# Performance work log

Measured on AMD Instinct MI355X. Metric: run time of the kernel, lower is better.

Reference implementation:

```python
import jax, jax.numpy as jnp
import numpy as np

B, S, D, H = 2, 4096, 768, 12
DEPTH = D // H


def setup_inputs() -> dict:
    key = jax.random.key(0)
    ks = jax.random.split(key, 6)
    return {
        "q": jax.random.normal(ks[0], (B, S, D), dtype=jnp.float32),
        "k": jax.random.normal(ks[1], (B, S, D), dtype=jnp.float32),
        "v": jax.random.normal(ks[2], (B, S, D), dtype=jnp.float32),
        "wq": jax.random.normal(ks[3], (D, D), dtype=jnp.float32),
        "wk": jax.random.normal(ks[4], (D, D), dtype=jnp.float32),
        "wv": jax.random.normal(ks[5], (D, D), dtype=jnp.float32),
    }


def _split_heads(x):
    # [B, S, D] -> [B, H, S, depth]
    b, s, _ = x.shape
    return x.reshape(b, s, H, DEPTH).transpose(0, 2, 1, 3)


def reference(q, k, v, wq, wk, wv):
    qh = _split_heads(q @ wq)  # [B,H,S,dh]
    kh = _split_heads(k @ wk)
    vh = _split_heads(v @ wv)
    scale = 1.0 / jnp.sqrt(jnp.asarray(DEPTH, dtype=qh.dtype))
    scores = jnp.einsum("bhqd,bhkd->bhqk", qh, kh) * scale  # [B,H,S,S]
    attn = jax.nn.softmax(scores, axis=-1)
    out = jnp.einsum("bhqk,bhkd->bhqd", attn, vh)  # [B,H,S,dh]
    return out.transpose(0, 2, 1, 3).reshape(q.shape[0], -1, D)
```

## Files before the change

kernel.cpp:

```cpp
#include <hip/hip_runtime.h>
#include <cstdint>

#define B_   2
#define S_   4096
#define D_   768
#define H_   12
#define DH_  64
#define BH_  (B_*H_)
#define M_   (B_*S_)
#define SCALE 0.125f

typedef _Float16 fp16;
typedef __attribute__((ext_vector_type(8))) _Float16 fp16x8;
typedef __attribute__((ext_vector_type(4))) _Float16 fp16x4;
typedef __attribute__((ext_vector_type(4))) float    f32x4;

#define MFMA16(a,b,c) __builtin_amdgcn_mfma_f32_16x16x32_f16((a),(b),(c),0,0,0)

__device__ __forceinline__ void gld_lds16(const void* g, void* l) {
  __builtin_amdgcn_global_load_lds(
      (const __attribute__((address_space(1))) unsigned int*)g,
      (__attribute__((address_space(3))) unsigned int*)l, 16, 0, 0);
}

__device__ __forceinline__ void stage64x128(const char* gbase, int pitch,
                                            char* lds, int tid) {
  const int lane = tid & 63, wv = tid >> 6;
#pragma unroll
  for (int j = 0; j < 2; ++j) {
    const int o   = (wv*2 + j)*1024 + lane*16;
    const int row = o >> 7;
    const int cb  = (o & 127) ^ ((row & 7) << 4);
    gld_lds16(gbase + (size_t)row*pitch + cb, lds + (wv*2 + j)*1024);
  }
}

__device__ __forceinline__ fp16x8 lds_h8(const char* base, int row, int cb) {
  return *(const fp16x8*)(base + row*128 + (cb ^ ((row & 7) << 4)));
}

__global__ __launch_bounds__(256) void prep_w(const float* __restrict__ wq,
                                              const float* __restrict__ wk,
                                              const float* __restrict__ wv,
                                              fp16* __restrict__ wt) {
  const int idx = blockIdx.x*256 + threadIdx.x;
  const int mat = idx / (768*768);
  const int e   = idx % (768*768);
  const int n   = e / 768, k = e % 768;
  const float* w = mat == 0 ? wq : (mat == 1 ? wk : wv);
  const float v = w[(size_t)k*768 + n];
  fp16* base = wt + (size_t)mat * (2*768*768);
  const fp16 hv = (fp16)v;
  base[e]            = hv;
  base[768*768 + e]  = (fp16)(v - (float)hv);
}

__global__ __launch_bounds__(256) void proj_gemm(
    const float* __restrict__ xq, const float* __restrict__ xk,
    const float* __restrict__ xv, const fp16* __restrict__ wt,
    fp16* __restrict__ qhi, fp16* __restrict__ qlo,
    fp16* __restrict__ khi, fp16* __restrict__ klo,
    fp16* __restrict__ vtp) {
  __shared__ __align__(16) char sm[16384];
  char* sWh = sm;
  char* sWl = sm + 8192;
  const int tid = threadIdx.x, lane = tid & 63, wv = tid >> 6;
  const int c = lane & 15, g = lane >> 4;
  const int mb  = blockIdx.x * 64;
  const int h   = blockIdx.y;
  const int nb  = h * 64;
  const int mat = blockIdx.z;
  const float* x = mat == 0 ? xq : (mat == 1 ? xk : xv);
  const fp16* wth = wt + (size_t)mat * (2*768*768);
  const fp16* wtl = wth + 768*768;

  f32x4 acc[4] = {};
  const int xrow = mb + wv*16 + c;

  for (int k0 = 0; k0 < 768; k0 += 64) {
    __syncthreads();
    stage64x128((const char*)(wth + (size_t)nb*768 + k0), 768*2, sWh, tid);
    stage64x128((const char*)(wtl + (size_t)nb*768 + k0), 768*2, sWl, tid);
    __syncthreads();

    fp16x8 ah[2], al[2];
#pragma unroll
    for (int ks = 0; ks < 2; ++ks) {
      const float* xp = x + (size_t)xrow*768 + k0 + ks*32 + g*8;
      const f32x4 x0 = *(const f32x4*)xp;
      const f32x4 x1 = *(const f32x4*)(xp + 4);
#pragma unroll
      for (int j = 0; j < 8; ++j) {
        const float v = j < 4 ? x0[j] : x1[j - 4];
        const fp16 hv = (fp16)v;
        ah[ks][j] = hv;
        al[ks][j] = (fp16)(v - (float)hv);
      }
    }
#pragma unroll
    for (int ks = 0; ks < 2; ++ks)
#pragma unroll
      for (int nt = 0; nt < 4; ++nt) {
        const fp16x8 bh = lds_h8(sWh, nt*16 + c, ks*64 + g*16);
        const fp16x8 bl = lds_h8(sWl, nt*16 + c, ks*64 + g*16);
        acc[nt] = MFMA16(ah[ks], bh, acc[nt]);
        acc[nt] = MFMA16(ah[ks], bl, acc[nt]);
        acc[nt] = MFMA16(al[ks], bh, acc[nt]);
      }
  }

  if (mat < 2) {
    fp16* ph = mat ? khi : qhi;
    fp16* pl = mat ? klo : qlo;
#pragma unroll
    for (int nt = 0; nt < 4; ++nt)
#pragma unroll
      for (int r = 0; r < 4; ++r) {
        const int m = mb + wv*16 + g*4 + r;
        const int bb = m >> 12, s = m & (S_-1);
        const size_t idx = ((size_t)(bb*H_ + h)*S_ + s)*DH_ + nt*16 + c;
        const float v = acc[nt][r];
        const fp16 hv = (fp16)v;
        ph[idx] = hv;
        pl[idx] = (fp16)(v - (float)hv);
      }
  } else {
    __syncthreads();
    fp16* tile = (fp16*)sm;
#pragma unroll
    for (int nt = 0; nt < 4; ++nt) {
      const int dd = nt*16 + c, ml = wv*16 + g*4;
      const fp16x4 hv = {(fp16)acc[nt][0], (fp16)acc[nt][1],
                         (fp16)acc[nt][2], (fp16)acc[nt][3]};
      *(fp16x4*)(tile + dd*64 + ml) = hv;
    }
    __syncthreads();
    const int bb = mb >> 12, s0 = mb & (S_-1);
    const int dd = tid >> 2, ml0 = (tid & 3) * 16;
    const size_t obase = ((size_t)(bb*H_ + h)*DH_ + dd)*S_ + s0 + ml0;
#pragma unroll
    for (int u = 0; u < 2; ++u)
      *(fp16x8*)(vtp + obase + u*8) = *(const fp16x8*)(tile + dd*64 + ml0 + u*8);
  }
}

__global__ __launch_bounds__(256) void mha_flash(
    const fp16* __restrict__ qhi, const fp16* __restrict__ qlo,
    const fp16* __restrict__ khi, const fp16* __restrict__ klo,
    const fp16* __restrict__ vt, float* __restrict__ out) {
  __shared__ __align__(16) char sm[49152];
  char* sQh = sm;
  char* sQl = sm + 8192;
  char* sKh = sm + 16384;
  char* sKl = sm + 24576;
  char* sV  = sm + 32768;
  char* sP  = sm + 40960;

  const int tid = threadIdx.x, lane = tid & 63, wv = tid >> 6;
  const int c = lane & 15, g = lane >> 4;
  const int qb = blockIdx.x * 64;
  const int bh = blockIdx.y;
  const int b = bh / H_, h = bh % H_;

  const size_t qoff = ((size_t)bh*S_ + qb) * DH_;
  stage64x128((const char*)(qhi + qoff), 128, sQh, tid);
  stage64x128((const char*)(qlo + qoff), 128, sQl, tid);
  __syncthreads();

  fp16x8 qfh[2], qfl[2];
#pragma unroll
  for (int ks = 0; ks < 2; ++ks) {
    qfh[ks] = lds_h8(sQh, wv*16 + c, ks*64 + g*16);
    qfl[ks] = lds_h8(sQl, wv*16 + c, ks*64 + g*16);
  }

  float m_run = -1e30f, l_run = 0.f;
  f32x4 accO[4] = {};

  for (int kt = 0; kt < S_/64; ++kt) {
    const int kvb = kt * 64;
    __syncthreads();
    const size_t koff = ((size_t)bh*S_ + kvb) * DH_;
    stage64x128((const char*)(khi + koff), 128, sKh, tid);
    stage64x128((const char*)(klo + koff), 128, sKl, tid);
    stage64x128((const char*)(vt + (size_t)bh*DH_*S_ + kvb), S_*2, sV, tid);
    __syncthreads();

    f32x4 accS[4] = {};
#pragma unroll
    for (int t = 0; t < 4; ++t)
#pragma unroll
      for (int ks = 0; ks < 2; ++ks) {
        const fp16x8 kfh = lds_h8(sKh, t*16 + c, ks*64 + g*16);
        const fp16x8 kfl = lds_h8(sKl, t*16 + c, ks*64 + g*16);
        accS[t] = MFMA16(kfh, qfh[ks], accS[t]);
        accS[t] = MFMA16(kfh, qfl[ks], accS[t]);
        accS[t] = MFMA16(kfl, qfh[ks], accS[t]);
      }

    float mx = -1e30f;
#pragma unroll
    for (int t = 0; t < 4; ++t)
#pragma unroll
      for (int r = 0; r < 4; ++r) mx = fmaxf(mx, accS[t][r]);
    mx = fmaxf(mx, __shfl_xor(mx, 16));
    mx = fmaxf(mx, __shfl_xor(mx, 32));
    const float m_new = fmaxf(m_run, mx);
    const float corr = __expf((m_run - m_new) * SCALE);
    float psum = 0.f;
#pragma unroll
    for (int t = 0; t < 4; ++t)
#pragma unroll
      for (int r = 0; r < 4; ++r) {
        const float p = __expf((accS[t][r] - m_new) * SCALE);
        accS[t][r] = p;
        psum += p;
      }
    psum += __shfl_xor(psum, 16);
    psum += __shfl_xor(psum, 32);
    l_run = l_run * corr + psum;
    m_run = m_new;

    char* pbase = sP + wv*2048;
#pragma unroll
    for (int t = 0; t < 4; ++t) {
      const fp16x4 pw = {(fp16)accS[t][0], (fp16)accS[t][1],
                         (fp16)accS[t][2], (fp16)accS[t][3]};
      *(fp16x4*)(pbase + c*128 + ((t*32 + g*8) ^ ((c & 7) << 4))) = pw;
    }

    float cr[4];
#pragma unroll
    for (int r = 0; r < 4; ++r)
      cr[r] = __shfl(corr, (lane & 48) | (g*4 + r));
#pragma unroll
    for (int d = 0; d < 4; ++d)
#pragma unroll
      for (int r = 0; r < 4; ++r) accO[d][r] *= cr[r];

#pragma unroll
    for (int ks = 0; ks < 2; ++ks) {
      const fp16x8 pf = *(const fp16x8*)(pbase + c*128 +
                                         ((ks*64 + g*16) ^ ((c & 7) << 4)));
#pragma unroll
      for (int d = 0; d < 4; ++d) {
        const fp16x8 vf = lds_h8(sV, d*16 + c, ks*64 + g*16);
        accO[d] = MFMA16(pf, vf, accO[d]);
      }
    }
  }

  float inv[4];
#pragma unroll
  for (int r = 0; r < 4; ++r)
    inv[r] = 1.f / __shfl(l_run, (lane & 48) | (g*4 + r));
  const int s0 = qb + wv*16 + g*4;
#pragma unroll
  for (int d = 0; d < 4; ++d)
#pragma unroll
    for (int r = 0; r < 4; ++r)
      out[((size_t)(b*S_ + s0 + r))*D_ + h*DH_ + d*16 + c] = accO[d][r] * inv[r];
}

extern "C" void kernel_launch(void* const* d_in, const int* in_sizes, int n_in,
                              void* d_out, int out_size, void* d_ws, size_t ws_size,
                              hipStream_t stream) {
  const float* xq = (const float*)d_in[0];
  const float* xk = (const float*)d_in[1];
  const float* xv = (const float*)d_in[2];
  const float* wq = (const float*)d_in[3];
  const float* wk = (const float*)d_in[4];
  const float* wv = (const float*)d_in[5];
  float* out = (float*)d_out;

  fp16* wt  = (fp16*)d_ws;
  fp16* qhi = wt + (size_t)6*768*768;
  const size_t PL = (size_t)BH_*S_*DH_;
  fp16* qlo = qhi + PL;
  fp16* khi = qlo + PL;
  fp16* klo = khi + PL;
  fp16* vtp = klo + PL;

  hipLaunchKernelGGL(prep_w, dim3(3*768*768/256), dim3(256), 0, stream,
                     wq, wk, wv, wt);
  hipLaunchKernelGGL(proj_gemm, dim3(M_/64, H_, 3), dim3(256), 0, stream,
                     xq, xk, xv, wt, qhi, qlo, khi, klo, vtp);
  hipLaunchKernelGGL(mha_flash, dim3(S_/64, BH_), dim3(256), 0, stream,
                     qhi, qlo, khi, klo, vtp, out);
}
```

Before: 524.2 us.

## Double query rows per flash block and streamline softmax with exp2 and lazy rescale

The attention kernel now handles 128 query rows per block (32 per wave) instead of 64, so each staged K/V tile is reused across twice as many queries. The grid is halved to match. Softmax switches to hardware exp2 with a pre-folded scale, packs probabilities with cvt_pkrtz, and skips the accumulator rescale when no row max grows. Row sums are computed with an MFMA against a ones vector instead of shuffles. LDS swizzle offsets are precomputed per lane. The costs are higher register pressure and fewer blocks per launch, and rounding the sum from fp16 P rather than fp32 slightly changes numerics.

```diff
diff --git a/kernel.cpp b/kernel.cpp
--- a/kernel.cpp
+++ b/kernel.cpp
@@ -8,7 +8,6 @@
 #define DH_  64
 #define BH_  (B_*H_)
 #define M_   (B_*S_)
-#define SCALE 0.125f
 
 typedef _Float16 fp16;
 typedef __attribute__((ext_vector_type(8))) _Float16 fp16x8;
@@ -16,6 +15,14 @@
 typedef __attribute__((ext_vector_type(4))) float    f32x4;
 
 #define MFMA16(a,b,c) __builtin_amdgcn_mfma_f32_16x16x32_f16((a),(b),(c),0,0,0)
+
+__device__ __forceinline__ float exp2_hw(float x) {
+  float r; asm("v_exp_f32 %0, %1" : "=v"(r) : "v"(x)); return r;
+}
+__device__ __forceinline__ uint32_t pkrtz(float a, float b) {
+  uint32_t r; asm("v_cvt_pkrtz_f16_f32 %0, %1, %2" : "=v"(r) : "v"(a), "v"(b));
+  return r;
+}
 
 __device__ __forceinline__ void gld_lds16(const void* g, void* l) {
   __builtin_amdgcn_global_load_lds(
@@ -33,10 +40,6 @@
     const int cb  = (o & 127) ^ ((row & 7) << 4);
     gld_lds16(gbase + (size_t)row*pitch + cb, lds + (wv*2 + j)*1024);
   }
-}
-
-__device__ __forceinline__ fp16x8 lds_h8(const char* base, int row, int cb) {
-  return *(const fp16x8*)(base + row*128 + (cb ^ ((row & 7) << 4)));
 }
 
 __global__ __launch_bounds__(256) void prep_w(const float* __restrict__ wq,
@@ -66,6 +69,9 @@
   char* sWl = sm + 8192;
   const int tid = threadIdx.x, lane = tid & 63, wv = tid >> 6;
   const int c = lane & 15, g = lane >> 4;
+  const int r128 = c * 128;
+  const int co0 = ((c & 7) ^ g) << 4;
+  const int co1 = co0 ^ 64;
   const int mb  = blockIdx.x * 64;
   const int h   = blockIdx.y;
   const int nb  = h * 64;
@@ -79,8 +85,8 @@
 
   for (int k0 = 0; k0 < 768; k0 += 64) {
     __syncthreads();
-    stage64x128((const char*)(wth + (size_t)nb*768 + k0), 768*2, sWh, tid);
-    stage64x128((const char*)(wtl + (size_t)nb*768 + k0), 768*2, sWl, tid);
+    stage64x128((const char*)(wth + (size_t)nb*768 + k0), 1536, sWh, tid);
+    stage64x128((const char*)(wtl + (size_t)nb*768 + k0), 1536, sWl, tid);
     __syncthreads();
 
     fp16x8 ah[2], al[2];
@@ -101,8 +107,11 @@
     for (int ks = 0; ks < 2; ++ks)
 #pragma unroll
       for (int nt = 0; nt < 4; ++nt) {
-        const fp16x8 bh = lds_h8(sWh, nt*16 + c, ks*64 + g*16);
-        const fp16x8 bl = lds_h8(sWl, nt*16 + c, ks*64 + g*16);
+        const char* wb  = sWh + r128 + nt*2048;
+        const char* wlb = sWl + r128 + nt*2048;
+        const int co = ks ? co1 : co0;
+        const fp16x8 bh = *(const fp16x8*)(wb  + co);
+        const fp16x8 bl = *(const fp16x8*)(wlb + co);
         acc[nt] = MFMA16(ah[ks], bh, acc[nt]);
         acc[nt] = MFMA16(ah[ks], bl, acc[nt]);
         acc[nt] = MFMA16(al[ks], bh, acc[nt]);
@@ -148,118 +157,169 @@
     const fp16* __restrict__ qhi, const fp16* __restrict__ qlo,
     const fp16* __restrict__ khi, const fp16* __restrict__ klo,
     const fp16* __restrict__ vt, float* __restrict__ out) {
-  __shared__ __align__(16) char sm[49152];
-  char* sQh = sm;
-  char* sQl = sm + 8192;
-  char* sKh = sm + 16384;
-  char* sKl = sm + 24576;
-  char* sV  = sm + 32768;
-  char* sP  = sm + 40960;
+  __shared__ __align__(16) char sm[40960];
+  char* sKh = sm;
+  char* sKl = sm + 8192;
+  char* sV  = sm + 16384;
+  char* sP  = sm + 24576;
 
   const int tid = threadIdx.x, lane = tid & 63, wv = tid >> 6;
   const int c = lane & 15, g = lane >> 4;
-  const int qb = blockIdx.x * 64;
+  const int r128 = c * 128;
+  const int co0 = ((c & 7) ^ g) << 4;
+  const int co1 = co0 ^ 64;
+  const int pg3 = (g & 1) << 3;
+  const int pse = ((c & 7) ^ (g >> 1)) << 4;
+  const int qb = blockIdx.x * 128;
   const int bh = blockIdx.y;
   const int b = bh / H_, h = bh % H_;
 
   const size_t qoff = ((size_t)bh*S_ + qb) * DH_;
-  stage64x128((const char*)(qhi + qoff), 128, sQh, tid);
-  stage64x128((const char*)(qlo + qoff), 128, sQl, tid);
+  stage64x128((const char*)(qhi + qoff),          128, sm,         tid);
+  stage64x128((const char*)(qhi + qoff + 64*DH_), 128, sm +  8192, tid);
+  stage64x128((const char*)(qlo + qoff),          128, sm + 16384, tid);
+  stage64x128((const char*)(qlo + qoff + 64*DH_), 128, sm + 24576, tid);
   __syncthreads();
 
-  fp16x8 qfh[2], qfl[2];
-#pragma unroll
-  for (int ks = 0; ks < 2; ++ks) {
-    qfh[ks] = lds_h8(sQh, wv*16 + c, ks*64 + g*16);
-    qfl[ks] = lds_h8(sQl, wv*16 + c, ks*64 + g*16);
-  }
-
-  float m_run = -1e30f, l_run = 0.f;
-  f32x4 accO[4] = {};
+  fp16x8 qfh[2][2], qfl[2][2];
+  {
+    const char* hb = sm + (wv >> 1)*8192;
+    const char* lb = sm + 16384 + (wv >> 1)*8192;
+#pragma unroll
+    for (int qs = 0; qs < 2; ++qs) {
+      const int rl = ((wv & 1)*32 + qs*16 + c) * 128;
+      qfh[qs][0] = *(const fp16x8*)(hb + rl + co0);
+      qfh[qs][1] = *(const fp16x8*)(hb + rl + co1);
+      qfl[qs][0] = *(const fp16x8*)(lb + rl + co0);
+      qfl[qs][1] = *(const fp16x8*)(lb + rl + co1);
+    }
+  }
+
+  float m_run[2] = {-1e30f, -1e30f};
+  float lrow[2][4] = {};
+  f32x4 accO[2][4] = {};
+  fp16x8 ones;
+#pragma unroll
+  for (int j = 0; j < 8; ++j) ones[j] = (fp16)1.0f;
+  const float C2 = 0.125f * 1.4426950408889634f;
 
   for (int kt = 0; kt < S_/64; ++kt) {
-    const int kvb = kt * 64;
-    __syncthreads();
-    const size_t koff = ((size_t)bh*S_ + kvb) * DH_;
+    __syncthreads();
+    const size_t koff = ((size_t)bh*S_ + kt*64) * DH_;
     stage64x128((const char*)(khi + koff), 128, sKh, tid);
     stage64x128((const char*)(klo + koff), 128, sKl, tid);
-    stage64x128((const char*)(vt + (size_t)bh*DH_*S_ + kvb), S_*2, sV, tid);
-    __syncthreads();
-
-    f32x4 accS[4] = {};
-#pragma unroll
-    for (int t = 0; t < 4; ++t)
-#pragma unroll
-      for (int ks = 0; ks < 2; ++ks) {
-        const fp16x8 kfh = lds_h8(sKh, t*16 + c, ks*64 + g*16);
-        const fp16x8 kfl = lds_h8(sKl, t*16 + c, ks*64 + g*16);
-        accS[t] = MFMA16(kfh, qfh[ks], accS[t]);
-        accS[t] = MFMA16(kfh, qfl[ks], accS[t]);
-        accS[t] = MFMA16(kfl, qfh[ks], accS[t]);
-      }
-
-    float mx = -1e30f;
-#pragma unroll
-    for (int t = 0; t < 4; ++t)
-#pragma unroll
-      for (int r = 0; r < 4; ++r) mx = fmaxf(mx, accS[t][r]);
-    mx = fmaxf(mx, __shfl_xor(mx, 16));
-    mx = fmaxf(mx, __shfl_xor(mx, 32));
-    const float m_new = fmaxf(m_run, mx);
-    const float corr = __expf((m_run - m_new) * SCALE);
-    float psum = 0.f;
-#pragma unroll
-    for (int t = 0; t < 4; ++t)
-#pragma unroll
-      for (int r = 0; r < 4; ++r) {
-        const float p = __expf((accS[t][r] - m_new) * SCALE);
-        accS[t][r] = p;
-        psum += p;
-      }
-    psum += __shfl_xor(psum, 16);
-    psum += __shfl_xor(psum, 32);
-    l_run = l_run * corr + psum;
-    m_run = m_new;
-
-    char* pbase = sP + wv*2048;
+    stage64x128((const char*)(vt + (size_t)bh*DH_*S_ + kt*64), S_*2, sV, tid);
+    __syncthreads();
+
+    f32x4 accS[2][4] = {};
 #pragma unroll
     for (int t = 0; t < 4; ++t) {
-      const fp16x4 pw = {(fp16)accS[t][0], (fp16)accS[t][1],
-                         (fp16)accS[t][2], (fp16)accS[t][3]};
-      *(fp16x4*)(pbase + c*128 + ((t*32 + g*8) ^ ((c & 7) << 4))) = pw;
-    }
-
-    float cr[4];
-#pragma unroll
-    for (int r = 0; r < 4; ++r)
-      cr[r] = __shfl(corr, (lane & 48) | (g*4 + r));
+      const char* kb = sKh + r128 + t*2048;
+      const char* lb = sKl + r128 + t*2048;
+      const fp16x8 kh0 = *(const fp16x8*)(kb + co0);
+      const fp16x8 kh1 = *(const fp16x8*)(kb + co1);
+      const fp16x8 kl0 = *(const fp16x8*)(lb + co0);
+      const fp16x8 kl1 = *(const fp16x8*)(lb + co1);
+#pragma unroll
+      for (int qs = 0; qs < 2; ++qs) {
+        accS[qs][t] = MFMA16(kh0, qfh[qs][0], accS[qs][t]);
+        accS[qs][t] = MFMA16(kh0, qfl[qs][0], accS[qs][t]);
+        accS[qs][t] = MFMA16(kl0, qfh[qs][0], accS[qs][t]);
+        accS[qs][t] = MFMA16(kh1, qfh[qs][1], accS[qs][t]);
+        accS[qs][t] = MFMA16(kh1, qfl[qs][1], accS[qs][t]);
+        accS[qs][t] = MFMA16(kl1, qfh[qs][1], accS[qs][t]);
+      }
+    }
+
+    float mx0 = -1e30f, mx1 = -1e30f;
+#pragma unroll
+    for (int t = 0; t < 4; ++t) {
+      mx0 = fmaxf(mx0, fmaxf(fmaxf(accS[0][t][0], accS[0][t][1]),
+                             fmaxf(accS[0][t][2], accS[0][t][3])));
+      mx1 = fmaxf(mx1, fmaxf(fmaxf(accS[1][t][0], accS[1][t][1]),
+                             fmaxf(accS[1][t][2], accS[1][t][3])));
+    }
+    mx0 = fmaxf(mx0, __shfl_xor(mx0, 16));
+    mx0 = fmaxf(mx0, __shfl_xor(mx0, 32));
+    mx1 = fmaxf(mx1, __shfl_xor(mx1, 16));
+    mx1 = fmaxf(mx1, __shfl_xor(mx1, 32));
+
+    const bool rec = (mx0 > m_run[0]) || (mx1 > m_run[1]);
+    if (__any(rec)) {
+#pragma unroll
+      for (int qs = 0; qs < 2; ++qs) {
+        const float mxq = qs ? mx1 : mx0;
+        const float m_new = fmaxf(m_run[qs], mxq);
+        const float corr = exp2_hw(__builtin_fmaf(m_run[qs], C2, -m_new*C2));
+        m_run[qs] = m_new;
+        float crow[4];
+#pragma unroll
+        for (int r = 0; r < 4; ++r)
+          crow[r] = __shfl(corr, (lane & 48) | (g*4 + r));
+#pragma unroll
+        for (int r = 0; r < 4; ++r) lrow[qs][r] *= crow[r];
+#pragma unroll
+        for (int d = 0; d < 4; ++d)
+#pragma unroll
+          for (int r = 0; r < 4; ++r) accO[qs][d][r] *= crow[r];
+      }
+    }
+
+    char* pbase = sP + wv*4096 + r128;
+#pragma unroll
+    for (int qs = 0; qs < 2; ++qs) {
+      const float negnm = -m_run[qs]*C2;
+      char* pb = pbase + qs*2048;
+#pragma unroll
+      for (int t = 0; t < 4; ++t) {
+        const float p0 = exp2_hw(__builtin_fmaf(accS[qs][t][0], C2, negnm));
+        const float p1 = exp2_hw(__builtin_fmaf(accS[qs][t][1], C2, negnm));
+        const float p2 = exp2_hw(__builtin_fmaf(accS[qs][t][2], C2, negnm));
+        const float p3 = exp2_hw(__builtin_fmaf(accS[qs][t][3], C2, negnm));
+        uint2 pw; pw.x = pkrtz(p0, p1); pw.y = pkrtz(p2, p3);
+        *(uint2*)(pb + (pg3 | (pse ^ (t*32)))) = pw;
+      }
+    }
+
+    const fp16x8 pA0 = *(const fp16x8*)(pbase + co0);
+    const fp16x8 pA1 = *(const fp16x8*)(pbase + co1);
+    const fp16x8 pB0 = *(const fp16x8*)(pbase + 2048 + co0);
+    const fp16x8 pB1 = *(const fp16x8*)(pbase + 2048 + co1);
+    f32x4 aL0 = {}, aL1 = {};
+    aL0 = MFMA16(pA0, ones, aL0);
+    aL0 = MFMA16(pA1, ones, aL0);
+    aL1 = MFMA16(pB0, ones, aL1);
+    aL1 = MFMA16(pB1, ones, aL1);
+#pragma unroll
+    for (int d = 0; d < 4; ++d) {
+      const char* vb = sV + r128 + d*2048;
+      const fp16x8 v0 = *(const fp16x8*)(vb + co0);
+      const fp16x8 v1 = *(const fp16x8*)(vb + co1);
+      accO[0][d] = MFMA16(pA0, v0, accO[0][d]);
+      accO[0][d] = MFMA16(pA1, v1, accO[0][d]);
+      accO[1][d] = MFMA16(pB0, v0, accO[1][d]);
+      accO[1][d] = MFMA16(pB1, v1, accO[1][d]);
+    }
+#pragma unroll
+    for (int r = 0; r < 4; ++r) {
+      lrow[0][r] += aL0[r];
+      lrow[1][r] += aL1[r];
+    }
+  }
+
+#pragma unroll
+  for (int qs = 0; qs < 2; ++qs) {
+    float inv[4];
+#pragma unroll
+    for (int r = 0; r < 4; ++r) inv[r] = 1.f / lrow[qs][r];
+    const int s0 = qb + wv*32 + qs*16 + g*4;
 #pragma unroll
     for (int d = 0; d < 4; ++d)
 #pragma unroll
-      for (int r = 0; r < 4; ++r) accO[d][r] *= cr[r];
-
-#pragma unroll
-    for (int ks = 0; ks < 2; ++ks) {
-      const fp16x8 pf = *(const fp16x8*)(pbase + c*128 +
-                                         ((ks*64 + g*16) ^ ((c & 7) << 4)));
-#pragma unroll
-      for (int d = 0; d < 4; ++d) {
-        const fp16x8 vf = lds_h8(sV, d*16 + c, ks*64 + g*16);
-        accO[d] = MFMA16(pf, vf, accO[d]);
-      }
-    }
-  }
-
-  float inv[4];
-#pragma unroll
-  for (int r = 0; r < 4; ++r)
-    inv[r] = 1.f / __shfl(l_run, (lane & 48) | (g*4 + r));
-  const int s0 = qb + wv*16 + g*4;
-#pragma unroll
-  for (int d = 0; d < 4; ++d)
-#pragma unroll
-    for (int r = 0; r < 4; ++r)
-      out[((size_t)(b*S_ + s0 + r))*D_ + h*DH_ + d*16 + c] = accO[d][r] * inv[r];
+      for (int r = 0; r < 4; ++r)
+        out[((size_t)(b*S_ + s0 + r))*D_ + h*DH_ + d*16 + c] =
+            accO[qs][d][r] * inv[r];
+  }
 }
 
 extern "C" void kernel_launch(void* const* d_in, const int* in_sizes, int n_in,
@@ -285,6 +345,6 @@
                      wq, wk, wv, wt);
   hipLaunchKernelGGL(proj_gemm, dim3(M_/64, H_, 3), dim3(256), 0, stream,
                      xq, xk, xv, wt, qhi, qlo, khi, klo, vtp);
-  hipLaunchKernelGGL(mha_flash, dim3(S_/64, BH_), dim3(256), 0, stream,
+  hipLaunchKernelGGL(mha_flash, dim3(S_/128, BH_), dim3(256), 0, stream,
                      qhi, qlo, khi, klo, vtp, out);
 }
```

New measurement: 514.5 us. Within noise of the previous version (-1.9%).
